# Optimization experiments

Measured on AMD Instinct MI355X. Metric: run time of the kernel, lower is better.

The kernel has to match this reference:

```python
import jax, jax.numpy as jnp
import numpy as np

SIGMA = 0.01        # config['fscore_sigma']
FSCORE_W = 0.1      # config['fscore_weight']
TASK_W = 1.0        # config['task_weight']
DOMAIN_W = 0.1      # config['domain_weight']


def setup_inputs() -> dict:
    key = jax.random.key(0)
    ks = jax.random.split(key, 11)
    B, N, M, F = 8, 4096, 4096, 512
    H1, H2, D = 256, 128, 6
    return {
        "pred_pc": jax.random.normal(ks[0], (B, N, 3), jnp.float32),
        "target_pc": jax.random.normal(ks[1], (B, M, 3), jnp.float32),
        "domain_features": jax.random.normal(ks[2], (B, F), jnp.float32),
        "dataset_weights": jax.random.uniform(ks[3], (B,), jnp.float32, 0.9, 1.2),
        "W1": jax.random.normal(ks[4], (F, H1), jnp.float32) * 0.02,
        "b1": jnp.zeros((H1,), jnp.float32),
        "W2": jax.random.normal(ks[5], (H1, H2), jnp.float32) * 0.02,
        "b2": jnp.zeros((H2,), jnp.float32),
        "W3": jax.random.normal(ks[6], (H2, D), jnp.float32) * 0.02,
        "b3": jnp.zeros((D,), jnp.float32),
        "domain_labels": jax.random.randint(ks[7], (B,), 0, D),
    }


def _chamfer_mins(pred, tgt):
    # pred: [B,N,3], tgt: [B,M,3] -> squared pairwise dists [B,N,M], then dual mins
    d = (jnp.sum(pred ** 2, axis=2)[:, :, None]
         + jnp.sum(tgt ** 2, axis=2)[:, None, :]
         - 2.0 * jnp.einsum('bnd,bmd->bnm', pred, tgt))
    return jnp.min(d, axis=2), jnp.min(d, axis=1)   # [B,N], [B,M]


def reference(pred_pc, target_pc, domain_features, dataset_weights,
              W1, b1, W2, b2, W3, b3, domain_labels):
    min_a, min_b = _chamfer_mins(pred_pc, target_pc)
    c = 2.0 * SIGMA * SIGMA
    soft_a = jnp.exp(-min_a / c)
    soft_b = jnp.exp(-min_b / c)

    # batch-level task loss (compute_reconstruction_loss on full batch)
    chamfer = jnp.mean(min_a) + jnp.mean(min_b)
    prec = jnp.mean(soft_a)
    rec = jnp.mean(soft_b)
    fscore = 2.0 * prec * rec / (prec + rec + 1e-8)
    task = chamfer + FSCORE_W * (1.0 - fscore)

    # per-sample dataset-weighted loss (vectorized form of the Python loop)
    ch_i = jnp.mean(min_a, axis=1) + jnp.mean(min_b, axis=1)
    p_i = jnp.mean(soft_a, axis=1)
    r_i = jnp.mean(soft_b, axis=1)
    f_i = 2.0 * p_i * r_i / (p_i + r_i + 1e-8)
    loss_i = ch_i + FSCORE_W * (1.0 - f_i)
    dataset_weighted = jnp.mean(dataset_weights * loss_i)

    # domain loss: GRL is identity in forward; classifier in eval mode (dropout off)
    h = jax.nn.relu(domain_features @ W1 + b1)
    h = jax.nn.relu(h @ W2 + b2)
    logits = h @ W3 + b3
    logp = jax.nn.log_softmax(logits, axis=-1)
    domain = -jnp.mean(jnp.take_along_axis(logp, domain_labels[:, None], axis=1))

    total = TASK_W * task + DOMAIN_W * domain + dataset_weighted
    return total
```

## Files before the change

### kernel.cpp

```cpp
#include <hip/hip_runtime.h>
#include <math.h>

#define B 8
#define NPTS 4096
#define QPT 8
#define THREADS 256

__device__ __forceinline__ float min3f(float a, float b, float c) {
  return fminf(fminf(a, b), c);
}


template<int S, int LOG2S>
__global__ __launch_bounds__(THREADS, 4) void k1_kernel(
    const float* __restrict__ pred, const float* __restrict__ targ,
    const float* __restrict__ x, const float* __restrict__ W1,
    float* __restrict__ partial, float* __restrict__ sums64,
    float* __restrict__ h1p) {
  constexpr int REFS = NPTS / S;
  const int id = blockIdx.x;
  const int tid = threadIdx.x;

  __shared__ float4 refs[REFS];
  __shared__ float xs[64];

  if (id < 64) {
    if (id == 0 && tid < 64) sums64[tid] = 0.f;
    int b = id >> 3, kc = id & 7;
    if (tid < 64) xs[tid] = x[b * 512 + kc * 64 + tid];
    __syncthreads();
    float acc = 0.f;
    const float* w = W1 + (size_t)(kc * 64) * 256 + tid;
#pragma unroll 8
    for (int k = 0; k < 64; ++k) acc = fmaf(xs[k], w[k * 256], acc);
    h1p[(b * 8 + kc) * 256 + tid] = acc;
    return;
  }

  int cid = id - 64;
  int split  = cid & (S - 1);
  int qchunk = (cid >> LOG2S) & 1;
  int b      = (cid >> (LOG2S + 1)) & 7;
  int dir    = cid >> (LOG2S + 4);
  const float* qp = dir ? targ : pred;
  const float* rp = dir ? pred : targ;

  const float* rb = rp + ((size_t)b * NPTS + (size_t)split * REFS) * 3;
  for (int i = tid; i < REFS; i += THREADS) {
    float xx = rb[i * 3 + 0], yy = rb[i * 3 + 1], zz = rb[i * 3 + 2];
    refs[i] = make_float4(xx, yy, zz, 0.5f * (xx * xx + yy * yy + zz * zz));
  }
  __syncthreads();

  const float* qb = qp + (size_t)b * NPTS * 3;
  int q0 = qchunk * (QPT * THREADS) + tid;
  float qx[QPT], qy[QPT], qz[QPT], vmin[QPT];
#pragma unroll
  for (int i = 0; i < QPT; ++i) {
    int q = q0 + i * THREADS;
    qx[i] = qb[q * 3 + 0];
    qy[i] = qb[q * 3 + 1];
    qz[i] = qb[q * 3 + 2];
    vmin[i] = 3.4e38f;
  }

  for (int j = 0; j < REFS; j += 8) {
    float4 t[8];
#pragma unroll
    for (int u = 0; u < 8; ++u) t[u] = refs[j + u];
#pragma unroll
    for (int i = 0; i < QPT; ++i) {
      float s[8];
#pragma unroll
      for (int u = 0; u < 8; ++u)
        s[u] = fmaf(-qx[i], t[u].x,
               fmaf(-qy[i], t[u].y, fmaf(-qz[i], t[u].z, t[u].w)));
      float m0 = min3f(s[0], s[1], s[2]);
      float m1 = min3f(s[3], s[4], s[5]);
      float m2 = min3f(s[6], s[7], m0);
      vmin[i] = min3f(m1, m2, vmin[i]);
    }
  }

  size_t base = (((size_t)dir * B + b) * S + split) * NPTS;
#pragma unroll
  for (int i = 0; i < QPT; ++i) {
    float qn = fmaf(qx[i], qx[i], fmaf(qy[i], qy[i], qz[i] * qz[i]));
    partial[base + q0 + i * THREADS] = fmaf(2.f, vmin[i], qn);
  }
}

template<int S>
__global__ __launch_bounds__(THREADS) void k2_kernel(
    const float* __restrict__ partial, float* __restrict__ sums64,
    const float* __restrict__ h1p, const float* __restrict__ b1,
    const float* __restrict__ W2, const float* __restrict__ b2,
    const float* __restrict__ W3, const float* __restrict__ b3,
    const int* __restrict__ labels, const float* __restrict__ wgt,
    float* __restrict__ out) {
  constexpr int NBLK = 272;
  const int id = blockIdx.x;
  const int tid = threadIdx.x;
  __shared__ float red[8];
  __shared__ float hs[128];
  __shared__ bool is_last;

  if (id >= 256) {
    int lid = id - 256;
    int b = lid >> 1, half = lid & 1;
    if (tid < 128) {
      int k = half * 128 + tid;
      float a = b1[k];
#pragma unroll
      for (int p = 0; p < 8; ++p) a += h1p[(b * 8 + p) * 256 + k];
      hs[tid] = fmaxf(a, 0.f);
    }
    __syncthreads();
    if (tid < 128) {
      float acc = 0.f;
      const float* w = W2 + (size_t)(half * 128) * 128 + tid;
#pragma unroll 8
      for (int k = 0; k < 128; ++k) acc = fmaf(hs[k], w[k * 128], acc);
      float* h2p = sums64 + 64 + 64 * 256;
      h2p[(b * 2 + half) * 128 + tid] = acc;
    }
    __threadfence();
    __syncthreads();
    if (tid == 0) {
      unsigned t = atomicAdd((unsigned*)(sums64 + 32), 1u);
      is_last = (t == NBLK - 1);
    }
  } else {
    int chunk = id & 15;
    int b   = (id >> 4) & 7;
    int dir = id >> 7;
    size_t pb = ((size_t)dir * B + b) * S * NPTS;
    int q = chunk * 256 + tid;

    float v[S];
#pragma unroll
    for (int s = 0; s < S; ++s)
      v[s] = partial[pb + (size_t)s * NPTS + q];
    float m = v[0];
#pragma unroll
    for (int s = 1; s < S; ++s) m = fminf(m, v[s]);
    float s_min = m;
    float s_soft = __expf(-5000.0f * m);

    for (int off = 32; off > 0; off >>= 1) {
      s_min  += __shfl_down(s_min,  off);
      s_soft += __shfl_down(s_soft, off);
    }
    int wave = tid >> 6, lane = tid & 63;
    if (lane == 0) { red[wave * 2] = s_min; red[wave * 2 + 1] = s_soft; }
    __syncthreads();
    if (tid == 0) {
      float a = 0.f, c = 0.f;
      for (int wv = 0; wv < 4; ++wv) { a += red[wv * 2]; c += red[wv * 2 + 1]; }
      atomicAdd(&sums64[(dir * B + b) * 2 + 0], a);
      atomicAdd(&sums64[(dir * B + b) * 2 + 1], c);
      asm volatile("s_waitcnt vmcnt(0)" ::: "memory");
      unsigned t = atomicAdd((unsigned*)(sums64 + 32), 1u);
      is_last = (t == NBLK - 1);
    }
  }
  __syncthreads();
  if (!is_last) return;
  __threadfence();

  __shared__ float h2s[8 * 128];
  __shared__ float lg[48];
  __shared__ float nlls[8];
  volatile const float* vh2 = (volatile const float*)(sums64 + 64 + 64 * 256);

  for (int i = tid; i < 1024; i += THREADS) {
    int bb = i >> 7, j = i & 127;
    float a = b2[j] + vh2[(bb * 2 + 0) * 128 + j] + vh2[(bb * 2 + 1) * 128 + j];
    h2s[i] = fmaxf(a, 0.f);
  }
  __syncthreads();
  if (tid < 48) {
    int bb = tid / 6, d = tid % 6;
    float acc = b3[d];
#pragma unroll 8
    for (int k = 0; k < 128; ++k)
      acc = fmaf(h2s[bb * 128 + k], W3[k * 6 + d], acc);
    lg[tid] = acc;
  }
  __syncthreads();
  if (tid < 8) {
    int bb = tid;
    float mx = lg[bb * 6];
    for (int d = 1; d < 6; ++d) mx = fmaxf(mx, lg[bb * 6 + d]);
    float se = 0.f;
    for (int d = 0; d < 6; ++d) se += __expf(lg[bb * 6 + d] - mx);
    int lab = labels[bb];
    nlls[bb] = -(lg[bb * 6 + lab] - mx - __logf(se));
  }
  __syncthreads();
  if (tid == 0) {
    volatile const float* vs = (volatile const float*)sums64;
    float chamfer = 0.f, prec = 0.f, rec = 0.f, dsw = 0.f, dom = 0.f;
    for (int bb = 0; bb < B; ++bb) {
      float sa  = vs[(0 * B + bb) * 2 + 0];
      float ssa = vs[(0 * B + bb) * 2 + 1];
      float sb  = vs[(1 * B + bb) * 2 + 0];
      float ssb = vs[(1 * B + bb) * 2 + 1];
      float ma = sa / 4096.f, mb = sb / 4096.f;
      float p = ssa / 4096.f, r = ssb / 4096.f;
      chamfer += ma + mb;
      prec += p; rec += r;
      float f_i = 2.f * p * r / (p + r + 1e-8f);
      float loss_i = ma + mb + 0.1f * (1.f - f_i);
      dsw += wgt[bb] * loss_i;
      dom += nlls[bb];
    }
    chamfer *= (1.f / B); prec *= (1.f / B); rec *= (1.f / B);
    dsw *= (1.f / B); dom *= (1.f / B);
    float fscore = 2.f * prec * rec / (prec + rec + 1e-8f);
    float task = chamfer + 0.1f * (1.f - fscore);
    out[0] = 1.0f * task + 0.1f * dom + dsw;
  }
}

template<int S, int LOG2S>
static void run_pipeline(const float* pred, const float* targ, const float* x,
                         const float* wgt, const float* W1, const float* b1,
                         const float* W2, const float* b2, const float* W3,
                         const float* b3, const int* labels, float* out,
                         char* ws, hipStream_t stream) {
  float* partial = (float*)ws;
  float* sums64  = partial + (size_t)2 * B * S * NPTS;
  float* h1p     = sums64 + 64;

  hipLaunchKernelGGL((k1_kernel<S, LOG2S>), dim3(64 + 32 * S), dim3(THREADS),
                     0, stream, pred, targ, x, W1, partial, sums64, h1p);
  hipLaunchKernelGGL((k2_kernel<S>), dim3(272), dim3(THREADS), 0, stream,
                     partial, sums64, h1p, b1, W2, b2, W3, b3, labels, wgt,
                     out);
}

extern "C" void kernel_launch(void* const* d_in, const int* in_sizes, int n_in,
                              void* d_out, int out_size, void* d_ws, size_t ws_size,
                              hipStream_t stream) {
  const float* pred   = (const float*)d_in[0];
  const float* targ   = (const float*)d_in[1];
  const float* x      = (const float*)d_in[2];
  const float* wgt    = (const float*)d_in[3];
  const float* W1     = (const float*)d_in[4];
  const float* b1     = (const float*)d_in[5];
  const float* W2     = (const float*)d_in[6];
  const float* b2     = (const float*)d_in[7];
  const float* W3     = (const float*)d_in[8];
  const float* b3     = (const float*)d_in[9];
  const int*   labels = (const int*)d_in[10];
  float* out = (float*)d_out;
  char* ws = (char*)d_ws;

  auto need = [](int S) {
    return ((size_t)2 * B * S * NPTS + 64 + 64 * 256 + 16 * 128) * sizeof(float);
  };
  if (ws_size >= need(32))
    run_pipeline<32, 5>(pred, targ, x, wgt, W1, b1, W2, b2, W3, b3, labels,
                        out, ws, stream);
  else if (ws_size >= need(16))
    run_pipeline<16, 4>(pred, targ, x, wgt, W1, b1, W2, b2, W3, b3, labels,
                        out, ws, stream);
  else
    run_pipeline<8, 3>(pred, targ, x, wgt, W1, b1, W2, b2, W3, b3, labels,
                       out, ws, stream);
}
```

Measured before the change: 118.2 us.

## Pack query pairs into v2f packed FMA/min and merge MLP blocks into chamfer blocks

The chamfer inner loop now handles two query points per packed float2 operation, using elementwise fma/min builtins so the compiler can emit packed FP32 instructions (v_pk_fma_f32). This is meant to halve the issued VALU instructions in the distance sweep. The first-layer MLP work for the domain classifier no longer gets 64 dedicated blocks; the first 64 chamfer blocks do it before their main work, so the grid shrinks. Query loads and norm computation are also moved ahead of the shared-memory barrier to overlap with the reference staging. Packed min may not map to a native packed instruction and could add overhead.

```diff
diff --git a/kernel.cpp b/kernel.cpp
--- a/kernel.cpp
+++ b/kernel.cpp
@@ -6,8 +6,29 @@
 #define QPT 8
 #define THREADS 256
 
+typedef float v2f __attribute__((ext_vector_type(2)));
+
 __device__ __forceinline__ float min3f(float a, float b, float c) {
   return fminf(fminf(a, b), c);
+}
+
+#if __has_builtin(__builtin_elementwise_fma)
+__device__ __forceinline__ v2f fma2(v2f a, v2f b, v2f c) {
+  return __builtin_elementwise_fma(a, b, c);
+}
+#else
+__device__ __forceinline__ v2f fma2(v2f a, v2f b, v2f c) {
+  v2f r; r.x = __builtin_fmaf(a.x, b.x, c.x); r.y = __builtin_fmaf(a.y, b.y, c.y);
+  return r;
+}
+#endif
+
+__device__ __forceinline__ v2f min2(v2f a, v2f b) {
+#if __has_builtin(__builtin_elementwise_min)
+  return __builtin_elementwise_min(a, b);
+#else
+  v2f r; r.x = fminf(a.x, b.x); r.y = fminf(a.y, b.y); return r;
+#endif
 }
 
 
@@ -34,14 +55,13 @@
 #pragma unroll 8
     for (int k = 0; k < 64; ++k) acc = fmaf(xs[k], w[k * 256], acc);
     h1p[(b * 8 + kc) * 256 + tid] = acc;
-    return;
-  }
-
-  int cid = id - 64;
-  int split  = cid & (S - 1);
-  int qchunk = (cid >> LOG2S) & 1;
-  int b      = (cid >> (LOG2S + 1)) & 7;
-  int dir    = cid >> (LOG2S + 4);
+    __syncthreads();
+  }
+
+  int split  = id & (S - 1);
+  int qchunk = (id >> LOG2S) & 1;
+  int b      = (id >> (LOG2S + 1)) & 7;
+  int dir    = id >> (LOG2S + 4);
   const float* qp = dir ? targ : pred;
   const float* rp = dir ? pred : targ;
 
@@ -50,43 +70,53 @@
     float xx = rb[i * 3 + 0], yy = rb[i * 3 + 1], zz = rb[i * 3 + 2];
     refs[i] = make_float4(xx, yy, zz, 0.5f * (xx * xx + yy * yy + zz * zz));
   }
-  __syncthreads();
 
   const float* qb = qp + (size_t)b * NPTS * 3;
   int q0 = qchunk * (QPT * THREADS) + tid;
-  float qx[QPT], qy[QPT], qz[QPT], vmin[QPT];
-#pragma unroll
-  for (int i = 0; i < QPT; ++i) {
-    int q = q0 + i * THREADS;
-    qx[i] = qb[q * 3 + 0];
-    qy[i] = qb[q * 3 + 1];
-    qz[i] = qb[q * 3 + 2];
-    vmin[i] = 3.4e38f;
-  }
+  float qn[QPT];
+  v2f nqx[QPT / 2], nqy[QPT / 2], nqz[QPT / 2], vmin2[QPT / 2];
+#pragma unroll
+  for (int p = 0; p < QPT / 2; ++p) {
+    int qa = q0 + (2 * p) * THREADS, qbi = q0 + (2 * p + 1) * THREADS;
+    float ax = qb[qa * 3 + 0], ay = qb[qa * 3 + 1], az = qb[qa * 3 + 2];
+    float bx = qb[qbi * 3 + 0], by = qb[qbi * 3 + 1], bz = qb[qbi * 3 + 2];
+    qn[2 * p]     = fmaf(ax, ax, fmaf(ay, ay, az * az));
+    qn[2 * p + 1] = fmaf(bx, bx, fmaf(by, by, bz * bz));
+    nqx[p] = (v2f){-ax, -bx};
+    nqy[p] = (v2f){-ay, -by};
+    nqz[p] = (v2f){-az, -bz};
+    vmin2[p] = (v2f){3.4e38f, 3.4e38f};
+  }
+  __syncthreads();
 
   for (int j = 0; j < REFS; j += 8) {
     float4 t[8];
 #pragma unroll
     for (int u = 0; u < 8; ++u) t[u] = refs[j + u];
 #pragma unroll
-    for (int i = 0; i < QPT; ++i) {
-      float s[8];
-#pragma unroll
-      for (int u = 0; u < 8; ++u)
-        s[u] = fmaf(-qx[i], t[u].x,
-               fmaf(-qy[i], t[u].y, fmaf(-qz[i], t[u].z, t[u].w)));
-      float m0 = min3f(s[0], s[1], s[2]);
-      float m1 = min3f(s[3], s[4], s[5]);
-      float m2 = min3f(s[6], s[7], m0);
-      vmin[i] = min3f(m1, m2, vmin[i]);
+    for (int p = 0; p < QPT / 2; ++p) {
+      v2f s[8];
+#pragma unroll
+      for (int u = 0; u < 8; ++u) {
+        v2f tx = (v2f){t[u].x, t[u].x};
+        v2f ty = (v2f){t[u].y, t[u].y};
+        v2f tz = (v2f){t[u].z, t[u].z};
+        v2f tw = (v2f){t[u].w, t[u].w};
+        s[u] = fma2(nqx[p], tx, fma2(nqy[p], ty, fma2(nqz[p], tz, tw)));
+      }
+      v2f m01 = min2(s[0], s[1]), m23 = min2(s[2], s[3]);
+      v2f m45 = min2(s[4], s[5]), m67 = min2(s[6], s[7]);
+      vmin2[p] = min2(vmin2[p], min2(min2(m01, m23), min2(m45, m67)));
     }
   }
 
   size_t base = (((size_t)dir * B + b) * S + split) * NPTS;
 #pragma unroll
-  for (int i = 0; i < QPT; ++i) {
-    float qn = fmaf(qx[i], qx[i], fmaf(qy[i], qy[i], qz[i] * qz[i]));
-    partial[base + q0 + i * THREADS] = fmaf(2.f, vmin[i], qn);
+  for (int p = 0; p < QPT / 2; ++p) {
+    partial[base + q0 + (2 * p) * THREADS] =
+        fmaf(2.f, vmin2[p].x, qn[2 * p]);
+    partial[base + q0 + (2 * p + 1) * THREADS] =
+        fmaf(2.f, vmin2[p].y, qn[2 * p + 1]);
   }
 }
 
@@ -233,7 +263,7 @@
   float* sums64  = partial + (size_t)2 * B * S * NPTS;
   float* h1p     = sums64 + 64;
 
-  hipLaunchKernelGGL((k1_kernel<S, LOG2S>), dim3(64 + 32 * S), dim3(THREADS),
+  hipLaunchKernelGGL((k1_kernel<S, LOG2S>), dim3(32 * S), dim3(THREADS),
                      0, stream, pred, targ, x, W1, partial, sums64, h1p);
   hipLaunchKernelGGL((k2_kernel<S>), dim3(272), dim3(THREADS), 0, stream,
                      partial, sums64, h1p, b1, W2, b2, W3, b3, labels, wgt,
```

New measurement: 119.0 us. No clear change (+0.7%).
